# Kernel optimization log

Measured on AMD Instinct MI355X. Metric: run time of the kernel, lower is better.

## Reference

```python
import jax, jax.numpy as jnp
import numpy as np

U, P, D, B, H = 8192, 4096, 64, 1024, 50
EPS = 1e-8  # torch.cosine_similarity eps


def setup_inputs() -> dict:
    key = jax.random.key(0)
    ks = jax.random.split(key, 11)
    inp = {}
    for i, name in enumerate(["A_up", "A_up_NR", "A_up_FR", "A_up_TR", "A_up_UR"]):
        inp[name] = jax.random.uniform(ks[i], (U, P), jnp.float32)
    inp["user_emb"] = jax.random.normal(ks[5], (U, D), jnp.float32) * 0.1
    inp["post_emb"] = jax.random.normal(ks[6], (P, D), jnp.float32) * 0.1
    inp["user_model"] = jax.random.normal(ks[7], (U, 4), jnp.float32)
    inp["X_source_id"] = jax.random.randint(ks[8], (B,), 0, P)
    inp["X_user_id"] = jax.random.randint(ks[9], (B,), 0, U)
    inp["X_rumer_id"] = jax.random.randint(ks[10], (B, H), 0, U)
    return inp


def _forward(A, user_emb, post_emb, W, X_source_id, X_rumer_id):
    # A: [5,U,P] stacked relations [base, NR, FR, TR, UR].
    # 2-layer LightGCN-style propagation, batched across all 5 relations:
    #   u_k = A @ p_{k-1};  p_k = A^T @ u_{k-1}
    u0, p0 = user_emb, post_emb
    u1 = jnp.einsum('rup,pd->rud', A, p0)    # [5,U,D]
    p1 = jnp.einsum('rup,ud->rpd', A, u0)    # [5,P,D]
    u2 = jnp.einsum('rup,rpd->rud', A, p1)
    p2 = jnp.einsum('rup,rud->rpd', A, u1)
    # fused stack+mean over the 3 layer outputs (x0, x1, x2)
    Xu = (u0[None] + u1 + u2) / 3.0          # [5,U,D]
    X_post_full = (p0 + p1[0] + p2[0]) / 3.0  # [P,D] (base relation only)

    base = Xu[0]   # [U,D]
    rel = Xu[1:]   # [4,U,D]

    # cosine similarity of base users vs each relation variant
    n0 = jnp.linalg.norm(base, axis=1)                # [U]
    nr = jnp.linalg.norm(rel, axis=2)                 # [4,U]
    sim = jnp.sum(base[None] * rel, axis=2) / jnp.maximum(n0[None] * nr, EPS)
    sim = sim.T                                       # [U,4]
    mask = (sim == sim.max(axis=1, keepdims=True)).astype(sim.dtype)
    simm = mask * sim
    var = jnp.log(jnp.std(simm, axis=1, ddof=1) + 1.0)  # [U]; torch.std is unbiased

    user = jnp.transpose(rel, (1, 0, 2))                 # [U,4,D]
    user_embedding = jnp.einsum('ua,uad->ud', W, user)   # [U,D]
    # note: post_embedding = A_pu @ user_embedding is computed in the original
    # get_Userembedding but never used by forward's outputs; omitted.

    X_post = X_post_full[X_source_id]                    # [B,D]
    Xvu = base[X_rumer_id]                               # [B,H,D]
    Xv = var[X_rumer_id]                                 # [B,H]
    X_var_user = jnp.einsum('bh,bhd->bd', Xv, Xvu)       # [B,D]
    AugUser = jnp.mean(user_embedding[X_rumer_id], axis=1)  # [B,D]
    X_mean_user = jnp.mean(Xvu, axis=1)                  # [B,D]
    return X_post, X_var_user, AugUser, X_mean_user


def reference(A_up, A_up_NR, A_up_FR, A_up_TR, A_up_UR,
              user_emb, post_emb, user_model,
              X_source_id, X_user_id, X_rumer_id):
    A = jnp.stack([A_up, A_up_NR, A_up_FR, A_up_TR, A_up_UR], axis=0)
    return _forward(A, user_emb, post_emb, user_model, X_source_id, X_rumer_id)
```

## Files before the change

### kernel.cpp

```cpp
#include <hip/hip_runtime.h>
#include <hip/hip_bf16.h>
#include <math.h>

#define U_DIM 8192
#define P_DIM 4096
#define D_DIM 64
#define B_DIM 1024
#define H_DIM 50
#define EPSV  1e-8f

typedef __attribute__((ext_vector_type(8))) short short8;
typedef __attribute__((ext_vector_type(4))) float f32x4;

struct APtrs { const float* p[5]; };

__device__ inline unsigned short f2bf(float f) {
    unsigned int u = __float_as_uint(f);
    u += 0x7FFFu + ((u >> 16) & 1u);
    return (unsigned short)(u >> 16);
}

template<bool TRANS>
__global__ __launch_bounds__(256) void gemm_n64(
    APtrs Aps, const float* Bmat, float* C,
    int M, int K, int ldm, long strideB, long strideC, int kseg)
{
    const int tid  = threadIdx.x;
    const int wid  = tid >> 6;
    const int lane = tid & 63;
    const int m0   = blockIdx.x * 128;
    const float* Ag = Aps.p[blockIdx.y];
    const float* Bp = Bmat + (size_t)blockIdx.y * strideB;
    float*       Cp = C    + (size_t)blockIdx.y * strideC;
    const int k_begin = blockIdx.z * kseg;
    const int k_end   = k_begin + kseg;

    __shared__ __align__(16) unsigned short a_s[128][40];
    __shared__ __align__(16) unsigned short b_s[64][40];

    f32x4 acc[2][4] = {};

    for (int kk = k_begin; kk < k_end; kk += 32) {
        if (!TRANS) {
            int row   = tid >> 1;
            int halfo = (tid & 1) << 4;
            const float* src = Ag + (size_t)(m0 + row) * K + kk + halfo;
            float4 v0 = ((const float4*)src)[0];
            float4 v1 = ((const float4*)src)[1];
            float4 v2 = ((const float4*)src)[2];
            float4 v3 = ((const float4*)src)[3];
            unsigned short* d = &a_s[row][halfo];
            d[0]=f2bf(v0.x); d[1]=f2bf(v0.y); d[2]=f2bf(v0.z); d[3]=f2bf(v0.w);
            d[4]=f2bf(v1.x); d[5]=f2bf(v1.y); d[6]=f2bf(v1.z); d[7]=f2bf(v1.w);
            d[8]=f2bf(v2.x); d[9]=f2bf(v2.y); d[10]=f2bf(v2.z); d[11]=f2bf(v2.w);
            d[12]=f2bf(v3.x); d[13]=f2bf(v3.y); d[14]=f2bf(v3.z); d[15]=f2bf(v3.w);
        } else {
            int krow = tid >> 3;
            int seg  = (tid & 7) << 4;
            const float* src = Ag + (size_t)(kk + krow) * ldm + m0 + seg;
            float4 v0 = ((const float4*)src)[0];
            float4 v1 = ((const float4*)src)[1];
            float4 v2 = ((const float4*)src)[2];
            float4 v3 = ((const float4*)src)[3];
            a_s[seg+ 0][krow]=f2bf(v0.x); a_s[seg+ 1][krow]=f2bf(v0.y);
            a_s[seg+ 2][krow]=f2bf(v0.z); a_s[seg+ 3][krow]=f2bf(v0.w);
            a_s[seg+ 4][krow]=f2bf(v1.x); a_s[seg+ 5][krow]=f2bf(v1.y);
            a_s[seg+ 6][krow]=f2bf(v1.z); a_s[seg+ 7][krow]=f2bf(v1.w);
            a_s[seg+ 8][krow]=f2bf(v2.x); a_s[seg+ 9][krow]=f2bf(v2.y);
            a_s[seg+10][krow]=f2bf(v2.z); a_s[seg+11][krow]=f2bf(v2.w);
            a_s[seg+12][krow]=f2bf(v3.x); a_s[seg+13][krow]=f2bf(v3.y);
            a_s[seg+14][krow]=f2bf(v3.z); a_s[seg+15][krow]=f2bf(v3.w);
        }
        {
            int krow = tid >> 3;
            int nseg = (tid & 7) << 3;
            const float* src = Bp + ((size_t)(kk + krow) << 6) + nseg;
            float4 v0 = ((const float4*)src)[0];
            float4 v1 = ((const float4*)src)[1];
            b_s[nseg+0][krow]=f2bf(v0.x); b_s[nseg+1][krow]=f2bf(v0.y);
            b_s[nseg+2][krow]=f2bf(v0.z); b_s[nseg+3][krow]=f2bf(v0.w);
            b_s[nseg+4][krow]=f2bf(v1.x); b_s[nseg+5][krow]=f2bf(v1.y);
            b_s[nseg+6][krow]=f2bf(v1.z); b_s[nseg+7][krow]=f2bf(v1.w);
        }
        __syncthreads();

        const int ko   = (lane >> 4) << 3;
        const int mrow = (wid << 5) + (lane & 15);
        short8 af0 = *(const short8*)&a_s[mrow][ko];
        short8 af1 = *(const short8*)&a_s[mrow + 16][ko];
#pragma unroll
        for (int nt = 0; nt < 4; ++nt) {
            short8 bf = *(const short8*)&b_s[(nt << 4) + (lane & 15)][ko];
            acc[0][nt] = __builtin_amdgcn_mfma_f32_16x16x32_bf16(af0, bf, acc[0][nt], 0, 0, 0);
            acc[1][nt] = __builtin_amdgcn_mfma_f32_16x16x32_bf16(af1, bf, acc[1][nt], 0, 0, 0);
        }
        __syncthreads();
    }

    const int col   = lane & 15;
    const int rbase = (lane >> 4) << 2;
#pragma unroll
    for (int mt = 0; mt < 2; ++mt)
#pragma unroll
        for (int nt = 0; nt < 4; ++nt)
#pragma unroll
            for (int i = 0; i < 4; ++i) {
                int row = m0 + (wid << 5) + (mt << 4) + rbase + i;
                atomicAdd(&Cp[((size_t)row << 6) + (nt << 4) + col], acc[mt][nt][i]);
            }
}

__device__ inline float wsum(float v) {
#pragma unroll
    for (int off = 32; off > 0; off >>= 1) v += __shfl_xor(v, off, 64);
    return v;
}

__global__ __launch_bounds__(256) void user_stats_k(
    const float* __restrict__ u0, const float* __restrict__ u1,
    const float* __restrict__ u2, const float* __restrict__ W,
    float* __restrict__ base_o, float* __restrict__ var_o, float* __restrict__ ue_o)
{
    int u    = blockIdx.x * 4 + (threadIdx.x >> 6);
    int lane = threadIdx.x & 63;
    size_t ud = ((size_t)u << 6) + lane;

    float b0 = u0[ud];
    float xu[5];
#pragma unroll
    for (int r = 0; r < 5; ++r)
        xu[r] = (b0 + u1[(size_t)r * U_DIM * 64 + ud] + u2[(size_t)r * U_DIM * 64 + ud]) * (1.0f / 3.0f);

    float base = xu[0];
    float n0 = sqrtf(wsum(base * base));
    float sim[4];
#pragma unroll
    for (int a = 0; a < 4; ++a) {
        float d  = wsum(base * xu[a + 1]);
        float nr = sqrtf(wsum(xu[a + 1] * xu[a + 1]));
        sim[a] = d / fmaxf(n0 * nr, EPSV);
    }
    float smax = fmaxf(fmaxf(sim[0], sim[1]), fmaxf(sim[2], sim[3]));
    float ssum = 0.0f;
    float simm[4];
#pragma unroll
    for (int a = 0; a < 4; ++a) { simm[a] = (sim[a] == smax) ? sim[a] : 0.0f; ssum += simm[a]; }
    float mean = ssum * 0.25f;
    float vs = 0.0f;
#pragma unroll
    for (int a = 0; a < 4; ++a) { float t = simm[a] - mean; vs += t * t; }
    vs *= (1.0f / 3.0f);
    float var = logf(sqrtf(vs) + 1.0f);

    float ue = 0.0f;
#pragma unroll
    for (int a = 0; a < 4; ++a) ue += W[((size_t)u << 2) + a] * xu[a + 1];

    base_o[ud] = base;
    ue_o[ud]   = ue;
    if (lane == 0) var_o[u] = var;
}

__global__ __launch_bounds__(256) void gather_k(
    const float* __restrict__ p0, const float* __restrict__ p1r0, const float* __restrict__ p2,
    const float* __restrict__ base, const float* __restrict__ var, const float* __restrict__ ue,
    const int* __restrict__ src_id, const int* __restrict__ rumer, float* __restrict__ out)
{
    int b    = blockIdx.x * 4 + (threadIdx.x >> 6);
    int lane = threadIdx.x & 63;

    int sp = src_id[b];
    size_t spd = ((size_t)sp << 6) + lane;
    out[((size_t)b << 6) + lane] = (p0[spd] + p1r0[spd] + p2[spd]) * (1.0f / 3.0f);

    float xv = 0.0f, xm = 0.0f, au = 0.0f;
    for (int h = 0; h < H_DIM; ++h) {
        int uu = rumer[b * H_DIM + h];
        size_t uud = ((size_t)uu << 6) + lane;
        float bv = base[uud];
        xv += var[uu] * bv;
        xm += bv;
        au += ue[uud];
    }
    out[((size_t)(B_DIM     + b) << 6) + lane] = xv;
    out[((size_t)(2 * B_DIM + b) << 6) + lane] = au * (1.0f / H_DIM);
    out[((size_t)(3 * B_DIM + b) << 6) + lane] = xm * (1.0f / H_DIM);
}

extern "C" void kernel_launch(void* const* d_in, const int* in_sizes, int n_in,
                              void* d_out, int out_size, void* d_ws, size_t ws_size,
                              hipStream_t stream)
{
    const float* u0 = (const float*)d_in[5];
    const float* p0 = (const float*)d_in[6];
    const float* W  = (const float*)d_in[7];
    const int* src   = (const int*)d_in[8];
    const int* rumer = (const int*)d_in[10];
    float* out = (float*)d_out;

    APtrs Ap;
    for (int r = 0; r < 5; ++r) Ap.p[r] = (const float*)d_in[r];

    float* u1   = (float*)d_ws;
    float* p1   = u1 + 5l * U_DIM * 64;
    float* p2   = p1 + 5l * P_DIM * 64;
    float* u2   = p2 + (long)P_DIM * 64;
    float* base = u2 + 5l * U_DIM * 64;
    float* var  = base + (long)U_DIM * 64;
    float* ue   = var + U_DIM;

    size_t zero_bytes = (size_t)(5l * U_DIM * 64 + 5l * P_DIM * 64 + (long)P_DIM * 64 + 5l * U_DIM * 64) * sizeof(float);
    hipMemsetAsync(d_ws, 0, zero_bytes, stream);

    gemm_n64<false><<<dim3(64, 5, 2), 256, 0, stream>>>(Ap, p0, u1, U_DIM, P_DIM, 0, 0, (long)U_DIM * 64, 2048);
    gemm_n64<true ><<<dim3(32, 5, 4), 256, 0, stream>>>(Ap, u0, p1, P_DIM, U_DIM, P_DIM, 0, (long)P_DIM * 64, 2048);
    gemm_n64<false><<<dim3(64, 5, 2), 256, 0, stream>>>(Ap, p1, u2, U_DIM, P_DIM, 0, (long)P_DIM * 64, (long)U_DIM * 64, 2048);
    gemm_n64<true ><<<dim3(32, 1, 8), 256, 0, stream>>>(Ap, u1, p2, P_DIM, U_DIM, P_DIM, 0, 0, 1024);

    user_stats_k<<<U_DIM / 4, 256, 0, stream>>>(u0, u1, u2, W, base, var, ue);
    gather_k<<<B_DIM / 4, 256, 0, stream>>>(p0, p1, p2, base, var, ue, src, rumer, out);
}
```

Measured before the change: 1.006 ms.

## Prefetch next K-tile into registers, pad shared memory, vectorize LDS stores, double split-K

The GEMM kernel now loads the next K-tile's A and B values into registers while the MFMA work on the current tile runs, overlapping global-memory latency with compute. Shared-memory tiles move to a padded flat layout (AROW) with vectorized short8/short4/short2 stores, replacing scattered 16-bit stores and reducing bank conflicts in the transposed path. The load mapping is reorganized and split-K is doubled, giving more blocks to fill the GPU at the cost of more atomic adds into the outputs. Launch bounds also request 4 blocks per SM, which may limit registers.

```diff
diff --git a/kernel.cpp b/kernel.cpp
--- a/kernel.cpp
+++ b/kernel.cpp
@@ -4,13 +4,16 @@
 
 #define U_DIM 8192
 #define P_DIM 4096
-#define D_DIM 64
 #define B_DIM 1024
 #define H_DIM 50
 #define EPSV  1e-8f
 
 typedef __attribute__((ext_vector_type(8))) short short8;
+typedef __attribute__((ext_vector_type(4))) short short4v;
+typedef __attribute__((ext_vector_type(2))) short short2v;
 typedef __attribute__((ext_vector_type(4))) float f32x4;
+
+#define AROW(m) ((m) * 40 + ((m) & ~7))
 
 struct APtrs { const float* p[5]; };
 
@@ -21,9 +24,9 @@
 }
 
 template<bool TRANS>
-__global__ __launch_bounds__(256) void gemm_n64(
+__global__ __launch_bounds__(256, 4) void gemm_n64(
     APtrs Aps, const float* Bmat, float* C,
-    int M, int K, int ldm, long strideB, long strideC, int kseg)
+    int K, int ldm, long strideB, long strideC, int kseg)
 {
     const int tid  = threadIdx.x;
     const int wid  = tid >> 6;
@@ -33,64 +36,82 @@
     const float* Bp = Bmat + (size_t)blockIdx.y * strideB;
     float*       Cp = C    + (size_t)blockIdx.y * strideC;
     const int k_begin = blockIdx.z * kseg;
-    const int k_end   = k_begin + kseg;
-
-    __shared__ __align__(16) unsigned short a_s[128][40];
-    __shared__ __align__(16) unsigned short b_s[64][40];
+
+    __shared__ __align__(16) unsigned short a_s[128 * 41];
+    __shared__ __align__(16) unsigned short b_s[64 * 41];
+
+    const float* ap;
+    if (!TRANS) ap = Ag + (size_t)(m0 + (tid >> 1)) * K + k_begin + ((tid & 1) << 4);
+    else        ap = Ag + (size_t)(k_begin + ((tid >> 5) << 2)) * ldm + m0 + ((tid & 31) << 2);
+    const float* bp = Bp + ((size_t)(k_begin + ((tid >> 4) << 1)) << 6) + ((tid & 15) << 2);
+
+    float4 ra[4], rb[2];
+    if (!TRANS) {
+#pragma unroll
+        for (int j = 0; j < 4; ++j) ra[j] = ((const float4*)ap)[j];
+    } else {
+#pragma unroll
+        for (int j = 0; j < 4; ++j) ra[j] = *(const float4*)(ap + (size_t)j * ldm);
+    }
+    rb[0] = *(const float4*)bp;
+    rb[1] = *(const float4*)(bp + 64);
 
     f32x4 acc[2][4] = {};
-
-    for (int kk = k_begin; kk < k_end; kk += 32) {
+    const int iters = kseg >> 5;
+
+    for (int it = 0; it < iters; ++it) {
         if (!TRANS) {
-            int row   = tid >> 1;
-            int halfo = (tid & 1) << 4;
-            const float* src = Ag + (size_t)(m0 + row) * K + kk + halfo;
-            float4 v0 = ((const float4*)src)[0];
-            float4 v1 = ((const float4*)src)[1];
-            float4 v2 = ((const float4*)src)[2];
-            float4 v3 = ((const float4*)src)[3];
-            unsigned short* d = &a_s[row][halfo];
-            d[0]=f2bf(v0.x); d[1]=f2bf(v0.y); d[2]=f2bf(v0.z); d[3]=f2bf(v0.w);
-            d[4]=f2bf(v1.x); d[5]=f2bf(v1.y); d[6]=f2bf(v1.z); d[7]=f2bf(v1.w);
-            d[8]=f2bf(v2.x); d[9]=f2bf(v2.y); d[10]=f2bf(v2.z); d[11]=f2bf(v2.w);
-            d[12]=f2bf(v3.x); d[13]=f2bf(v3.y); d[14]=f2bf(v3.z); d[15]=f2bf(v3.w);
+            const int row = tid >> 1, ho = (tid & 1) << 4;
+            const float* f = (const float*)ra;
+            short8 w0, w1;
+#pragma unroll
+            for (int j = 0; j < 8; ++j) { w0[j] = (short)f2bf(f[j]); w1[j] = (short)f2bf(f[8 + j]); }
+            unsigned short* d = a_s + AROW(row) + ho;
+            *(short8*)d = w0;
+            *(short8*)(d + 8) = w1;
         } else {
-            int krow = tid >> 3;
-            int seg  = (tid & 7) << 4;
-            const float* src = Ag + (size_t)(kk + krow) * ldm + m0 + seg;
-            float4 v0 = ((const float4*)src)[0];
-            float4 v1 = ((const float4*)src)[1];
-            float4 v2 = ((const float4*)src)[2];
-            float4 v3 = ((const float4*)src)[3];
-            a_s[seg+ 0][krow]=f2bf(v0.x); a_s[seg+ 1][krow]=f2bf(v0.y);
-            a_s[seg+ 2][krow]=f2bf(v0.z); a_s[seg+ 3][krow]=f2bf(v0.w);
-            a_s[seg+ 4][krow]=f2bf(v1.x); a_s[seg+ 5][krow]=f2bf(v1.y);
-            a_s[seg+ 6][krow]=f2bf(v1.z); a_s[seg+ 7][krow]=f2bf(v1.w);
-            a_s[seg+ 8][krow]=f2bf(v2.x); a_s[seg+ 9][krow]=f2bf(v2.y);
-            a_s[seg+10][krow]=f2bf(v2.z); a_s[seg+11][krow]=f2bf(v2.w);
-            a_s[seg+12][krow]=f2bf(v3.x); a_s[seg+13][krow]=f2bf(v3.y);
-            a_s[seg+14][krow]=f2bf(v3.z); a_s[seg+15][krow]=f2bf(v3.w);
+            const int bm = tid & 31, bk = tid >> 5;
+            const float* f = (const float*)ra;
+#pragma unroll
+            for (int jm = 0; jm < 4; ++jm) {
+                short4v w = { (short)f2bf(f[jm]),     (short)f2bf(f[4 + jm]),
+                              (short)f2bf(f[8 + jm]), (short)f2bf(f[12 + jm]) };
+                *(short4v*)(a_s + AROW((bm << 2) + jm) + (bk << 2)) = w;
+            }
         }
         {
-            int krow = tid >> 3;
-            int nseg = (tid & 7) << 3;
-            const float* src = Bp + ((size_t)(kk + krow) << 6) + nseg;
-            float4 v0 = ((const float4*)src)[0];
-            float4 v1 = ((const float4*)src)[1];
-            b_s[nseg+0][krow]=f2bf(v0.x); b_s[nseg+1][krow]=f2bf(v0.y);
-            b_s[nseg+2][krow]=f2bf(v0.z); b_s[nseg+3][krow]=f2bf(v0.w);
-            b_s[nseg+4][krow]=f2bf(v1.x); b_s[nseg+5][krow]=f2bf(v1.y);
-            b_s[nseg+6][krow]=f2bf(v1.z); b_s[nseg+7][krow]=f2bf(v1.w);
+            const int bd = tid & 15, bk2 = tid >> 4;
+            const float* f = (const float*)rb;
+#pragma unroll
+            for (int jd = 0; jd < 4; ++jd) {
+                short2v w = { (short)f2bf(f[jd]), (short)f2bf(f[4 + jd]) };
+                *(short2v*)(b_s + AROW((bd << 2) + jd) + (bk2 << 1)) = w;
+            }
         }
         __syncthreads();
+
+        if (it + 1 < iters) {
+            if (!TRANS) {
+                ap += 32;
+#pragma unroll
+                for (int j = 0; j < 4; ++j) ra[j] = ((const float4*)ap)[j];
+            } else {
+                ap += (size_t)32 * ldm;
+#pragma unroll
+                for (int j = 0; j < 4; ++j) ra[j] = *(const float4*)(ap + (size_t)j * ldm);
+            }
+            bp += 32 * 64;
+            rb[0] = *(const float4*)bp;
+            rb[1] = *(const float4*)(bp + 64);
+        }
 
         const int ko   = (lane >> 4) << 3;
         const int mrow = (wid << 5) + (lane & 15);
-        short8 af0 = *(const short8*)&a_s[mrow][ko];
-        short8 af1 = *(const short8*)&a_s[mrow + 16][ko];
+        short8 af0 = *(const short8*)(a_s + AROW(mrow) + ko);
+        short8 af1 = *(const short8*)(a_s + AROW(mrow + 16) + ko);
 #pragma unroll
         for (int nt = 0; nt < 4; ++nt) {
-            short8 bf = *(const short8*)&b_s[(nt << 4) + (lane & 15)][ko];
+            short8 bf = *(const short8*)(b_s + AROW((nt << 4) + (lane & 15)) + ko);
             acc[0][nt] = __builtin_amdgcn_mfma_f32_16x16x32_bf16(af0, bf, acc[0][nt], 0, 0, 0);
             acc[1][nt] = __builtin_amdgcn_mfma_f32_16x16x32_bf16(af1, bf, acc[1][nt], 0, 0, 0);
         }
@@ -212,10 +233,10 @@
     size_t zero_bytes = (size_t)(5l * U_DIM * 64 + 5l * P_DIM * 64 + (long)P_DIM * 64 + 5l * U_DIM * 64) * sizeof(float);
     hipMemsetAsync(d_ws, 0, zero_bytes, stream);
 
-    gemm_n64<false><<<dim3(64, 5, 2), 256, 0, stream>>>(Ap, p0, u1, U_DIM, P_DIM, 0, 0, (long)U_DIM * 64, 2048);
-    gemm_n64<true ><<<dim3(32, 5, 4), 256, 0, stream>>>(Ap, u0, p1, P_DIM, U_DIM, P_DIM, 0, (long)P_DIM * 64, 2048);
-    gemm_n64<false><<<dim3(64, 5, 2), 256, 0, stream>>>(Ap, p1, u2, U_DIM, P_DIM, 0, (long)P_DIM * 64, (long)U_DIM * 64, 2048);
-    gemm_n64<true ><<<dim3(32, 1, 8), 256, 0, stream>>>(Ap, u1, p2, P_DIM, U_DIM, P_DIM, 0, 0, 1024);
+    gemm_n64<false><<<dim3(64, 5, 4), 256, 0, stream>>>(Ap, p0, u1, P_DIM, 0, 0, (long)U_DIM * 64, 1024);
+    gemm_n64<true ><<<dim3(32, 5, 8), 256, 0, stream>>>(Ap, u0, p1, U_DIM, P_DIM, 0, (long)P_DIM * 64, 1024);
+    gemm_n64<false><<<dim3(64, 5, 4), 256, 0, stream>>>(Ap, p1, u2, P_DIM, 0, (long)P_DIM * 64, (long)U_DIM * 64, 1024);
+    gemm_n64<true ><<<dim3(32, 1, 16), 256, 0, stream>>>(Ap, u1, p2, U_DIM, P_DIM, 0, 0, 512);
 
     user_stats_k<<<U_DIM / 4, 256, 0, stream>>>(u0, u1, u2, W, base, var, ue);
     gather_k<<<B_DIM / 4, 256, 0, stream>>>(p0, p1, p2, base, var, ue, src, rumer, out);
```

Result: faster. 889.2 us (-11.6%).
